# Kernel tuning notes

Measured on AMD Instinct MI355X. Metric: run time of the kernel, lower is better.

The kernel has to match this reference:

```python
import jax, jax.numpy as jnp
import numpy as np

D_MODEL = 1024
NUM_HEADS = 16
HEAD_DIM = D_MODEL // NUM_HEADS


def setup_inputs() -> dict:
    key = jax.random.key(0)
    ks = jax.random.split(key, 5)
    scale = 0.02
    return {
        "x": jax.random.normal(ks[0], (1, 4096, D_MODEL), dtype=jnp.float32),
        "w_qkv": jax.random.normal(ks[1], (D_MODEL, 3 * D_MODEL), dtype=jnp.float32) * scale,
        "b_qkv": jax.random.normal(ks[2], (3 * D_MODEL,), dtype=jnp.float32) * scale,
        "w_out": jax.random.normal(ks[3], (D_MODEL, D_MODEL), dtype=jnp.float32) * scale,
        "b_out": jax.random.normal(ks[4], (D_MODEL,), dtype=jnp.float32) * scale,
    }


def reference(x, w_qkv, b_qkv, w_out, b_out):
    B, S, D = x.shape
    H, Hd = NUM_HEADS, HEAD_DIM
    qkv = x @ w_qkv + b_qkv  # [B,S,3D]
    q, k, v = jnp.split(qkv, 3, axis=-1)
    # [B,H,S,Hd]
    q = q.reshape(B, S, H, Hd).transpose(0, 2, 1, 3)
    k = k.reshape(B, S, H, Hd).transpose(0, 2, 1, 3)
    v = v.reshape(B, S, H, Hd).transpose(0, 2, 1, 3)
    scores = jnp.einsum("bhqd,bhkd->bhqk", q, k) / jnp.sqrt(jnp.float32(Hd))
    causal = jnp.tril(jnp.ones((S, S), dtype=bool))
    scores = jnp.where(causal[None, None, :, :], scores, -jnp.inf)
    attn = jax.nn.softmax(scores, axis=-1)  # dropout_p = 0.0 -> identity
    ctx = jnp.einsum("bhqk,bhkd->bhqd", attn, v)
    ctx = ctx.transpose(0, 2, 1, 3).reshape(B, S, D)
    return ctx @ w_out + b_out
```

## Files before the change

### kernel.cpp

```cpp
#include <hip/hip_runtime.h>

#define S 4096
#define DM 1024
#define NH 16
#define HD 64

typedef __attribute__((ext_vector_type(8))) short bf8;
typedef __attribute__((ext_vector_type(4))) float f4;
typedef __attribute__((ext_vector_type(4))) short s4;
typedef __attribute__((ext_vector_type(4))) unsigned int u4;

#define MFMA __builtin_amdgcn_mfma_f32_16x16x32_bf16

#define QSCALE 0.18033688011112042f

static __device__ __forceinline__ unsigned short f2b(float f) {
  unsigned int u = __builtin_bit_cast(unsigned int, f);
  u += 0x7fffu + ((u >> 16) & 1u);
  return (unsigned short)(u >> 16);
}
static __device__ __forceinline__ float b2f(unsigned short u) {
  return __builtin_bit_cast(float, (unsigned int)u << 16);
}

static __device__ __forceinline__ void gld_lds(const unsigned short* g, unsigned short* l) {
  __builtin_amdgcn_global_load_lds(
      (const __attribute__((address_space(1))) unsigned int*)g,
      (__attribute__((address_space(3))) unsigned int*)l, 16, 0, 0);
}

__global__ void prep(const float* __restrict__ x, const float* __restrict__ w_qkv,
                     const float* __restrict__ w_out,
                     unsigned short* __restrict__ xb, unsigned short* __restrict__ wqkvT,
                     unsigned short* __restrict__ woutT) {
  __shared__ float tile[64][65];
  int b = blockIdx.x, t = threadIdx.x;
  if (b < 4096) {
    int i = (b * 256 + t) * 4;
    float4 v = *(const float4*)(x + i);
    s4 o;
    o.x = (short)f2b(v.x); o.y = (short)f2b(v.y);
    o.z = (short)f2b(v.z); o.w = (short)f2b(v.w);
    *(s4*)(xb + i) = o;
    return;
  }
  const float* in; unsigned short* out; int R, C, tc, tr;
  if (b < 4096 + 768) { int bb = b - 4096; in = w_qkv; out = wqkvT; R = DM; C = 3 * DM; tc = bb % 48; tr = bb / 48; }
  else                { int bb = b - 4864; in = w_out; out = woutT; R = DM; C = DM;     tc = bb % 16; tr = bb / 16; }
  int c = t & 63, rbase = (t >> 6) * 16;
#pragma unroll
  for (int i = 0; i < 16; i++) {
    int r = rbase + i;
    tile[r][c] = in[(tr * 64 + r) * C + tc * 64 + c];
  }
  __syncthreads();
#pragma unroll
  for (int i = 0; i < 16; i++) {
    int cc = rbase + i;
    out[(tc * 64 + cc) * R + tr * 64 + c] = f2b(tile[c][cc]);
  }
}


__global__ void __launch_bounds__(256, 2) gemm_qkv(const unsigned short* __restrict__ A,
                                                   const unsigned short* __restrict__ Bt,
                                                   const float* __restrict__ bias,
                                                   unsigned short* __restrict__ Qo,
                                                   unsigned short* __restrict__ Ko,
                                                   unsigned short* __restrict__ Vt) {
  __shared__ unsigned short lA[128 * 64];
  __shared__ unsigned short lB[128 * 64];
  int bid = blockIdx.x;
  int nb = bid % 24, mb = bid / 24;
  int m0 = mb * 128, n0 = nb * 128;
  int t = threadIdx.x, w = t >> 6, lane = t & 63;
  int col = lane & 15, quad = lane >> 4;
  int wm = (w >> 1) * 64, wn = (w & 1) * 64;

  int srow = lane >> 3;
  int sphys = lane & 7;

  f4 acc[4][4];
#pragma unroll
  for (int x = 0; x < 4; x++)
#pragma unroll
    for (int y = 0; y < 4; y++) acc[x][y] = (f4){0.f, 0.f, 0.f, 0.f};

  for (int k0 = 0; k0 < DM; k0 += 64) {
    __syncthreads();
#pragma unroll
    for (int p = 0; p < 4; p++) {
      int j = 4 * w + p;
      int row = j * 8 + srow;
      int lch = sphys ^ (row & 7);
      gld_lds(A + (size_t)(m0 + row) * DM + k0 + lch * 8, lA + j * 512);
      gld_lds(Bt + (size_t)(n0 + row) * DM + k0 + lch * 8, lB + j * 512);
    }
    __syncthreads();

#pragma unroll
    for (int ks = 0; ks < 2; ks++) {
      bf8 af[4], bfr[4];
      int sw = col & 7;
#pragma unroll
      for (int x = 0; x < 4; x++) {
        int rA = wm + x * 16 + col;
        af[x] = *(const bf8*)(lA + rA * 64 + ((quad + 4 * ks) ^ sw) * 8);
        int rB = wn + x * 16 + col;
        bfr[x] = *(const bf8*)(lB + rB * 64 + ((quad + 4 * ks) ^ sw) * 8);
      }
#pragma unroll
      for (int x = 0; x < 4; x++)
#pragma unroll
        for (int y = 0; y < 4; y++)
          acc[x][y] = MFMA(af[x], bfr[y], acc[x][y], 0, 0, 0);
    }
  }

#pragma unroll
  for (int x = 0; x < 4; x++) {
    int s0r = m0 + wm + x * 16 + quad * 4;
#pragma unroll
    for (int y = 0; y < 4; y++) {
      f4 a = acc[x][y];
      int n = n0 + wn + y * 16 + col;
      float bv = bias[n];
      if (n < 2048) {
        unsigned short* dst = (n < 1024) ? Qo : Ko;
        float sc = (n < 1024) ? QSCALE : 1.0f;
        int nn = n & 1023;
        int hh = nn >> 6, d = nn & 63;
        unsigned short* pp = dst + ((size_t)hh * S + s0r) * HD + d;
#pragma unroll
        for (int r = 0; r < 4; r++) pp[r * HD] = f2b((a[r] + bv) * sc);
      } else {
        int nn = n - 2048;
        int hh = nn >> 6, d = nn & 63;
        s4 pk;
        pk.x = (short)f2b(a[0] + bv);
        pk.y = (short)f2b(a[1] + bv);
        pk.z = (short)f2b(a[2] + bv);
        pk.w = (short)f2b(a[3] + bv);
        *(s4*)(Vt + ((size_t)hh * HD + d) * S + s0r) = pk;
      }
    }
  }
}

__global__ void __launch_bounds__(256, 2) gemm_out(const unsigned short* __restrict__ A,
                                                   const unsigned short* __restrict__ Bt,
                                                   const float* __restrict__ bias,
                                                   float* __restrict__ out) {
  __shared__ unsigned short lA[64 * 64];
  __shared__ unsigned short lB[128 * 64];
  int bid = blockIdx.x;
  int nb = bid % 8, mb = bid / 8;
  int m0 = mb * 64, n0 = nb * 128;
  int t = threadIdx.x, w = t >> 6, lane = t & 63;
  int col = lane & 15, quad = lane >> 4;
  int wm = (w >> 1) * 32, wn = (w & 1) * 64;

  int srow = lane >> 3;
  int sphys = lane & 7;

  f4 acc[2][4];
#pragma unroll
  for (int x = 0; x < 2; x++)
#pragma unroll
    for (int y = 0; y < 4; y++) acc[x][y] = (f4){0.f, 0.f, 0.f, 0.f};

  for (int k0 = 0; k0 < DM; k0 += 64) {
    __syncthreads();
#pragma unroll
    for (int p = 0; p < 2; p++) {
      int j = 2 * w + p;
      int row = j * 8 + srow;
      int lch = sphys ^ (row & 7);
      gld_lds(A + (size_t)(m0 + row) * DM + k0 + lch * 8, lA + j * 512);
    }
#pragma unroll
    for (int p = 0; p < 4; p++) {
      int j = 4 * w + p;
      int row = j * 8 + srow;
      int lch = sphys ^ (row & 7);
      gld_lds(Bt + (size_t)(n0 + row) * DM + k0 + lch * 8, lB + j * 512);
    }
    __syncthreads();

#pragma unroll
    for (int ks = 0; ks < 2; ks++) {
      bf8 af[2], bfr[4];
      int sw = col & 7;
#pragma unroll
      for (int x = 0; x < 2; x++) {
        int rA = wm + x * 16 + col;
        af[x] = *(const bf8*)(lA + rA * 64 + ((quad + 4 * ks) ^ sw) * 8);
      }
#pragma unroll
      for (int y = 0; y < 4; y++) {
        int rB = wn + y * 16 + col;
        bfr[y] = *(const bf8*)(lB + rB * 64 + ((quad + 4 * ks) ^ sw) * 8);
      }
#pragma unroll
      for (int x = 0; x < 2; x++)
#pragma unroll
        for (int y = 0; y < 4; y++)
          acc[x][y] = MFMA(af[x], bfr[y], acc[x][y], 0, 0, 0);
    }
  }

#pragma unroll
  for (int x = 0; x < 2; x++) {
    int s0r = m0 + wm + x * 16 + quad * 4;
#pragma unroll
    for (int y = 0; y < 4; y++) {
      f4 a = acc[x][y];
      int n = n0 + wn + y * 16 + col;
      float bv = bias[n];
#pragma unroll
      for (int r = 0; r < 4; r++) out[(size_t)(s0r + r) * DM + n] = a[r] + bv;
    }
  }
}

__global__ void __launch_bounds__(128, 4) attn(const unsigned short* __restrict__ Q,
                                               const unsigned short* __restrict__ K,
                                               const unsigned short* __restrict__ Vt,
                                               unsigned short* __restrict__ slabA,
                                               unsigned short* __restrict__ slab1,
                                               unsigned short* __restrict__ slab2,
                                               unsigned short* __restrict__ slab3,
                                               float* __restrict__ l0_g,
                                               float* __restrict__ l1_g,
                                               float* __restrict__ l2_g,
                                               float* __restrict__ l3_g) {
  __shared__ unsigned short kbuf[64 * 64];
  __shared__ unsigned short vbuf[64 * 64];

  int bid = blockIdx.x;
  int xcd = bid & 7;
  int kk = bid >> 3;
  int h = xcd + ((kk >= 160) ? 8 : 0);
  int cidx = (kk >= 160) ? (kk - 160) : kk;
  int j = 159 - cidx;
  int qb, c0, nst, p;
  if (j < 16) {
    qb = j; c0 = 0; nst = qb + 1; p = 0;
  } else if (j < 64) {
    int u = j - 16;
    qb = 16 + (u >> 1);
    int half = u & 1;
    int ntot = qb + 1, nh = (ntot + 1) >> 1;
    p = half;
    if (half) { c0 = nh; nst = ntot - nh; }
    else      { c0 = 0;  nst = nh; }
  } else {
    int u = j - 64;
    qb = 40 + (u >> 2);
    int qt = u & 3;
    int ntot = qb + 1;
    int base = ntot >> 2, rem = ntot & 3;
    c0 = qt * base + (qt < rem ? qt : rem);
    nst = base + (qt < rem ? 1 : 0);
    p = qt;
  }
  bool single = (qb < 16);
  int q0blk = qb * 64;
  int t = threadIdx.x, w = t >> 6, lane = t & 63;
  int col = lane & 15, quad = lane >> 4;
  int q0 = q0blk + w * 32;

  const unsigned short* Qh = Q + (size_t)h * S * HD;
  const unsigned short* Kh = K + (size_t)h * S * HD;
  const unsigned short* Vh = Vt + (size_t)h * HD * S;

  bf8 qf[2][2];
#pragma unroll
  for (int g = 0; g < 2; g++) {
    qf[g][0] = *(const bf8*)(Qh + (q0 + g * 16 + col) * HD + quad * 8);
    qf[g][1] = *(const bf8*)(Qh + (q0 + g * 16 + col) * HD + 32 + quad * 8);
  }

  f4 o[2][4];
#pragma unroll
  for (int g = 0; g < 2; g++)
#pragma unroll
    for (int dt = 0; dt < 4; dt++) o[g][dt] = (f4){0.f, 0.f, 0.f, 0.f};
  float lsum[2] = {0.f, 0.f};

  int srow = lane >> 3;
  int sphys = lane & 7;

  for (int s_ = 0; s_ < nst; s_++) {
    int kv0 = (c0 + s_) * 64;
    __syncthreads();
#pragma unroll
    for (int pp = 0; pp < 4; pp++) {
      int jj = 4 * w + pp;
      int row = jj * 8 + srow;
      int lch = sphys ^ (row & 7);
      gld_lds(Kh + (size_t)(kv0 + row) * HD + lch * 8, kbuf + jj * 512);
      gld_lds(Vh + (size_t)row * S + kv0 + lch * 8, vbuf + jj * 512);
    }
    __syncthreads();

    f4 st[2][4];
#pragma unroll
    for (int tt = 0; tt < 4; tt++) {
      int kr = tt * 16 + col;
      int sw = col & 7;
      bf8 ka = *(const bf8*)(kbuf + kr * 64 + (quad ^ sw) * 8);
      bf8 kb = *(const bf8*)(kbuf + kr * 64 + ((quad + 4) ^ sw) * 8);
#pragma unroll
      for (int g = 0; g < 2; g++) {
        f4 z = {0.f, 0.f, 0.f, 0.f};
        z = MFMA(ka, qf[g][0], z, 0, 0, 0);
        z = MFMA(kb, qf[g][1], z, 0, 0, 0);
        st[g][tt] = z;
      }
    }

#pragma unroll
    for (int g = 0; g < 2; g++) {
      int q16 = q0 + g * 16;
      if (kv0 + 63 > q16) {
        int q = q16 + col;
#pragma unroll
        for (int tt = 0; tt < 4; tt++)
#pragma unroll
          for (int rr = 0; rr < 4; rr++) {
            int kv = kv0 + tt * 16 + quad * 4 + rr;
            st[g][tt][rr] = (kv <= q) ? st[g][tt][rr] : -1e30f;
          }
      }
    }

    bf8 pf[2][2];
#pragma unroll
    for (int g = 0; g < 2; g++) {
      float pv[4][4];
#pragma unroll
      for (int tt = 0; tt < 4; tt++) {
#pragma unroll
        for (int rr = 0; rr < 4; rr++) pv[tt][rr] = __builtin_amdgcn_exp2f(st[g][tt][rr]);
        lsum[g] += (pv[tt][0] + pv[tt][1]) + (pv[tt][2] + pv[tt][3]);
      }
#pragma unroll
      for (int f = 0; f < 2; f++) {
        unsigned int a0, a1, b0, b1;
        asm("v_cvt_pk_bf16_f32 %0, %1, %2" : "=v"(a0) : "v"(pv[2 * f][0]),     "v"(pv[2 * f][1]));
        asm("v_cvt_pk_bf16_f32 %0, %1, %2" : "=v"(a1) : "v"(pv[2 * f][2]),     "v"(pv[2 * f][3]));
        asm("v_cvt_pk_bf16_f32 %0, %1, %2" : "=v"(b0) : "v"(pv[2 * f + 1][0]), "v"(pv[2 * f + 1][1]));
        asm("v_cvt_pk_bf16_f32 %0, %1, %2" : "=v"(b1) : "v"(pv[2 * f + 1][2]), "v"(pv[2 * f + 1][3]));
        asm("v_permlane32_swap_b32 %0, %1" : "+v"(a0), "+v"(b0));
        asm("v_permlane32_swap_b32 %0, %1" : "+v"(a1), "+v"(b1));
        asm("v_permlane16_swap_b32 %0, %1" : "+v"(a0), "+v"(b0));
        asm("v_permlane16_swap_b32 %0, %1" : "+v"(a1), "+v"(b1));
        u4 pk;
        pk.x = a0; pk.y = a1; pk.z = b0; pk.w = b1;
        pf[g][f] = __builtin_bit_cast(bf8, pk);
      }
    }

#pragma unroll
    for (int dt = 0; dt < 4; dt++) {
      int vr = dt * 16 + col;
      int sw = col & 7;
      bf8 v0 = *(const bf8*)(vbuf + vr * 64 + (quad ^ sw) * 8);
      bf8 v1 = *(const bf8*)(vbuf + vr * 64 + ((quad + 4) ^ sw) * 8);
#pragma unroll
      for (int g = 0; g < 2; g++) {
        o[g][dt] = MFMA(pf[g][0], v0, o[g][dt], 0, 0, 0);
        o[g][dt] = MFMA(pf[g][1], v1, o[g][dt], 0, 0, 0);
      }
    }
  }

#pragma unroll
  for (int g = 0; g < 2; g++) {
    float ls = lsum[g];
    ls += __shfl_xor(ls, 16);
    ls += __shfl_xor(ls, 32);
    int q16 = q0 + g * 16;
    if (single) {
      float inv = 1.0f / ls;
      float ir[4];
#pragma unroll
      for (int rr = 0; rr < 4; rr++) ir[rr] = __shfl(inv, quad * 4 + rr);
#pragma unroll
      for (int dt = 0; dt < 4; dt++)
#pragma unroll
        for (int rr = 0; rr < 4; rr++) {
          int row = q16 + quad * 4 + rr;
          slabA[(size_t)row * DM + h * HD + dt * 16 + col] = f2b(o[g][dt][rr] * ir[rr]);
        }
    } else {
      unsigned short* slab; int rowbase; float* lg;
      if (p == 0)      { slab = slabA; rowbase = q16;        lg = l0_g; }
      else if (p == 1) { slab = slab1; rowbase = q16 - 1024; lg = l1_g; }
      else if (p == 2) { slab = slab2; rowbase = q16 - 2560; lg = l2_g; }
      else             { slab = slab3; rowbase = q16 - 2560; lg = l3_g; }
      if (quad == 0) lg[h * S + q16 + col] = ls;
#pragma unroll
      for (int dt = 0; dt < 4; dt++)
#pragma unroll
        for (int rr = 0; rr < 4; rr++) {
          int row = rowbase + quad * 4 + rr;
          slab[(size_t)row * DM + h * HD + dt * 16 + col] = f2b(o[g][dt][rr]);
        }
    }
  }
}

__global__ void combine(unsigned short* __restrict__ Ctx,
                        const unsigned short* __restrict__ slab1,
                        const unsigned short* __restrict__ slab2,
                        const unsigned short* __restrict__ slab3,
                        const float* __restrict__ l0_g,
                        const float* __restrict__ l1_g,
                        const float* __restrict__ l2_g,
                        const float* __restrict__ l3_g) {
  int row = 1024 + blockIdx.x;
  int cc = threadIdx.x * 4;
  int h = cc >> 6;
  s4 a = *(const s4*)(Ctx + (size_t)row * DM + cc);
  s4 b = *(const s4*)(slab1 + (size_t)(row - 1024) * DM + cc);
  float acc0 = b2f((unsigned short)a.x) + b2f((unsigned short)b.x);
  float acc1 = b2f((unsigned short)a.y) + b2f((unsigned short)b.y);
  float acc2 = b2f((unsigned short)a.z) + b2f((unsigned short)b.z);
  float acc3 = b2f((unsigned short)a.w) + b2f((unsigned short)b.w);
  float l = l0_g[h * S + row] + l1_g[h * S + row];
  if (row >= 2560) {
    s4 c = *(const s4*)(slab2 + (size_t)(row - 2560) * DM + cc);
    s4 d = *(const s4*)(slab3 + (size_t)(row - 2560) * DM + cc);
    acc0 += b2f((unsigned short)c.x) + b2f((unsigned short)d.x);
    acc1 += b2f((unsigned short)c.y) + b2f((unsigned short)d.y);
    acc2 += b2f((unsigned short)c.z) + b2f((unsigned short)d.z);
    acc3 += b2f((unsigned short)c.w) + b2f((unsigned short)d.w);
    l += l2_g[h * S + row] + l3_g[h * S + row];
  }
  float inv = 1.0f / l;
  s4 o;
  o.x = (short)f2b(acc0 * inv);
  o.y = (short)f2b(acc1 * inv);
  o.z = (short)f2b(acc2 * inv);
  o.w = (short)f2b(acc3 * inv);
  *(s4*)(Ctx + (size_t)row * DM + cc) = o;
}

extern "C" void kernel_launch(void* const* d_in, const int* in_sizes, int n_in,
                              void* d_out, int out_size, void* d_ws, size_t ws_size,
                              hipStream_t stream) {
  const float* x     = (const float*)d_in[0];
  const float* w_qkv = (const float*)d_in[1];
  const float* b_qkv = (const float*)d_in[2];
  const float* w_out = (const float*)d_in[3];
  const float* b_out = (const float*)d_in[4];
  float* out = (float*)d_out;

  char* ws = (char*)d_ws;
  unsigned short* xb    = (unsigned short*)(ws);
  unsigned short* wqkvT = (unsigned short*)(ws + (size_t)8  * 1048576);
  unsigned short* woutT = (unsigned short*)(ws + (size_t)14 * 1048576);
  unsigned short* Qb    = (unsigned short*)(ws + (size_t)16 * 1048576);
  unsigned short* Kb    = (unsigned short*)(ws + (size_t)24 * 1048576);
  unsigned short* Vtb   = (unsigned short*)(ws + (size_t)32 * 1048576);
  unsigned short* ctx   = (unsigned short*)(ws + (size_t)40 * 1048576);

  unsigned short* slab1 = xb;
  float* l0_g = (float*)(ws + (size_t)6 * 1048576);
  float* l1_g = (float*)(ws + (size_t)6 * 1048576 + 256 * 1024);
  float* l2_g = (float*)(ws + (size_t)6 * 1048576 + 512 * 1024);
  float* l3_g = (float*)(ws + (size_t)6 * 1048576 + 768 * 1024);
  unsigned short* slab2 = wqkvT;
  unsigned short* slab3 = (unsigned short*)(ws + (size_t)11 * 1048576);

  prep<<<5120, 256, 0, stream>>>(x, w_qkv, w_out, xb, wqkvT, woutT);
  gemm_qkv<<<32 * 24, 256, 0, stream>>>(xb, wqkvT, b_qkv, Qb, Kb, Vtb);
  attn<<<NH * 160, 128, 0, stream>>>(Qb, Kb, Vtb, ctx, slab1, slab2, slab3,
                                     l0_g, l1_g, l2_g, l3_g);
  combine<<<3072, 256, 0, stream>>>(ctx, slab1, slab2, slab3, l0_g, l1_g, l2_g, l3_g);
  gemm_out<<<64 * 8, 256, 0, stream>>>(ctx, woutT, b_out, out);
}
```

Before: 194.0 us.

## Load K and V fragments directly from global memory instead of via LDS

Drops the shared-memory staging of K and V tiles, along with both block barriers per KV step. Each wave now loads its MFMA operand fragments for K and V straight from global memory into registers, and issues the V loads early to overlap with the softmax. This removes the barrier stalls and LDS traffic, but the waves of a block no longer share loads, so global and L2 traffic rises and register pressure grows.

Measured after the change: 311.0 us. +60.3%, slower.

```diff
diff --git a/kernel.cpp b/kernel.cpp
--- a/kernel.cpp
+++ b/kernel.cpp
@@ -234,9 +234,6 @@
                                                float* __restrict__ l1_g,
                                                float* __restrict__ l2_g,
                                                float* __restrict__ l3_g) {
-  __shared__ unsigned short kbuf[64 * 64];
-  __shared__ unsigned short vbuf[64 * 64];
-
   int bid = blockIdx.x;
   int xcd = bid & 7;
   int kk = bid >> 3;
@@ -288,36 +285,35 @@
     for (int dt = 0; dt < 4; dt++) o[g][dt] = (f4){0.f, 0.f, 0.f, 0.f};
   float lsum[2] = {0.f, 0.f};
 
-  int srow = lane >> 3;
-  int sphys = lane & 7;
-
   for (int s_ = 0; s_ < nst; s_++) {
     int kv0 = (c0 + s_) * 64;
-    __syncthreads();
-#pragma unroll
-    for (int pp = 0; pp < 4; pp++) {
-      int jj = 4 * w + pp;
-      int row = jj * 8 + srow;
-      int lch = sphys ^ (row & 7);
-      gld_lds(Kh + (size_t)(kv0 + row) * HD + lch * 8, kbuf + jj * 512);
-      gld_lds(Vh + (size_t)row * S + kv0 + lch * 8, vbuf + jj * 512);
-    }
-    __syncthreads();
+
+    bf8 ka[4], kb[4];
+#pragma unroll
+    for (int tt = 0; tt < 4; tt++) {
+      const unsigned short* kp = Kh + (size_t)(kv0 + tt * 16 + col) * HD;
+      ka[tt] = *(const bf8*)(kp + quad * 8);
+      kb[tt] = *(const bf8*)(kp + 32 + quad * 8);
+    }
 
     f4 st[2][4];
 #pragma unroll
     for (int tt = 0; tt < 4; tt++) {
-      int kr = tt * 16 + col;
-      int sw = col & 7;
-      bf8 ka = *(const bf8*)(kbuf + kr * 64 + (quad ^ sw) * 8);
-      bf8 kb = *(const bf8*)(kbuf + kr * 64 + ((quad + 4) ^ sw) * 8);
 #pragma unroll
       for (int g = 0; g < 2; g++) {
         f4 z = {0.f, 0.f, 0.f, 0.f};
-        z = MFMA(ka, qf[g][0], z, 0, 0, 0);
-        z = MFMA(kb, qf[g][1], z, 0, 0, 0);
+        z = MFMA(ka[tt], qf[g][0], z, 0, 0, 0);
+        z = MFMA(kb[tt], qf[g][1], z, 0, 0, 0);
         st[g][tt] = z;
       }
+    }
+
+    bf8 v0[4], v1[4];
+#pragma unroll
+    for (int dt = 0; dt < 4; dt++) {
+      const unsigned short* vp = Vh + (size_t)(dt * 16 + col) * S + kv0;
+      v0[dt] = *(const bf8*)(vp + quad * 8);
+      v1[dt] = *(const bf8*)(vp + 32 + quad * 8);
     }
 
 #pragma unroll
@@ -364,14 +360,10 @@
 
 #pragma unroll
     for (int dt = 0; dt < 4; dt++) {
-      int vr = dt * 16 + col;
-      int sw = col & 7;
-      bf8 v0 = *(const bf8*)(vbuf + vr * 64 + (quad ^ sw) * 8);
-      bf8 v1 = *(const bf8*)(vbuf + vr * 64 + ((quad + 4) ^ sw) * 8);
 #pragma unroll
       for (int g = 0; g < 2; g++) {
-        o[g][dt] = MFMA(pf[g][0], v0, o[g][dt], 0, 0, 0);
-        o[g][dt] = MFMA(pf[g][1], v1, o[g][dt], 0, 0, 0);
+        o[g][dt] = MFMA(pf[g][0], v0[dt], o[g][dt], 0, 0, 0);
+        o[g][dt] = MFMA(pf[g][1], v1[dt], o[g][dt], 0, 0, 0);
       }
     }
   }
```
